# Performance work log

Measured on AMD Instinct MI355X. Metric: run time of the kernel, lower is better.

The kernel has to match this reference:

```python
import jax, jax.numpy as jnp
import numpy as np

DIM = 1024
DEPTH = 2
D_STATE = 16
EXPAND = 2            # standard Mamba expand factor -> d_inner = 2*dim
D_CONV = 4
DT_RANK = DIM // 16   # ceil(dim/16) = 64
D_INNER = DIM * EXPAND
BATCH = 2
SEQ = 1024


def setup_inputs() -> dict:
    key = jax.random.key(0)
    ks = jax.random.split(key, 8)
    def n(k, shape, scale):
        return jax.random.normal(k, shape, jnp.float32) * scale
    # A_log initialized as log(1..N) per channel (S4D-real init, as in mamba_ssm)
    A_log = jnp.tile(jnp.log(jnp.arange(1, D_STATE + 1, dtype=jnp.float32))[None, None, :],
                     (DEPTH, D_INNER, 1))
    return {
        "x": n(ks[0], (BATCH, SEQ, DIM), 1.0),
        "in_proj_w": n(ks[1], (DEPTH, 2 * D_INNER, DIM), DIM ** -0.5),
        "conv_w": n(ks[2], (DEPTH, D_INNER, D_CONV), D_CONV ** -0.5),
        "conv_b": jnp.zeros((DEPTH, D_INNER), jnp.float32),
        "x_proj_w": n(ks[3], (DEPTH, DT_RANK + 2 * D_STATE, D_INNER), D_INNER ** -0.5),
        "dt_proj_w": n(ks[4], (DEPTH, D_INNER, DT_RANK), DT_RANK ** -0.5),
        "dt_proj_b": n(ks[5], (DEPTH, D_INNER), 0.1),
        "A_log": A_log,
        "D": jnp.ones((DEPTH, D_INNER), jnp.float32),
        "out_proj_w": n(ks[6], (DEPTH, DIM, D_INNER), D_INNER ** -0.5),
    }


def _mamba_layer(x, in_w, cw, cb, xp_w, dtw, dtb, A_log, Dp, ow):
    # x: [B, L, dim]
    Bsz = x.shape[0]
    xz = jnp.einsum('bld,ed->ble', x, in_w)            # [B, L, 2*d_inner]
    xi, z = jnp.split(xz, 2, axis=-1)
    # causal depthwise conv1d over time
    xc = jnp.transpose(xi, (0, 2, 1))                  # [B, d_inner, L]
    xc = jax.lax.conv_general_dilated(xc, cw[:, None, :], (1,), [(D_CONV - 1, 0)],
                                      feature_group_count=D_INNER)
    xc = xc + cb[None, :, None]
    xc = jax.nn.silu(jnp.transpose(xc, (0, 2, 1)))     # [B, L, d_inner]
    # input-dependent dt, B, C
    x_dbl = jnp.einsum('bld,ed->ble', xc, xp_w)        # [B, L, dt_rank+2*N]
    dt_raw = x_dbl[..., :DT_RANK]
    Bm = x_dbl[..., DT_RANK:DT_RANK + D_STATE]         # [B, L, N]
    Cm = x_dbl[..., DT_RANK + D_STATE:]                # [B, L, N]
    dt = jax.nn.softplus(jnp.einsum('blr,dr->bld', dt_raw, dtw) + dtb)  # [B, L, d_inner]
    A = -jnp.exp(A_log)                                # [d_inner, N]
    dA = jnp.exp(dt[..., None] * A[None, None])        # [B, L, d_inner, N]
    dBu = dt[..., None] * Bm[:, :, None, :] * xc[..., None]

    def step(h, inp):
        dA_t, dBu_t, C_t = inp
        h = dA_t * h + dBu_t                           # [B, d_inner, N]
        y = jnp.einsum('bdn,bn->bd', h, C_t)
        return h, y

    h0 = jnp.zeros((Bsz, D_INNER, D_STATE), x.dtype)
    _, ys = jax.lax.scan(step, h0,
                         (dA.transpose(1, 0, 2, 3), dBu.transpose(1, 0, 2, 3),
                          Cm.transpose(1, 0, 2)))
    y = ys.transpose(1, 0, 2) + Dp[None, None, :] * xc
    y = y * jax.nn.silu(z)
    return jnp.einsum('bld,od->blo', y, ow)


def reference(x, in_proj_w, conv_w, conv_b, x_proj_w, dt_proj_w, dt_proj_b, A_log, D, out_proj_w):
    for i in range(DEPTH):
        x = _mamba_layer(x, in_proj_w[i], conv_w[i], conv_b[i], x_proj_w[i],
                         dt_proj_w[i], dt_proj_b[i], A_log[i], D[i], out_proj_w[i])
    return x
```

## Files before the change

kernel.cpp:

```cpp
#include <hip/hip_runtime.h>
#include <hip/hip_bf16.h>

typedef __hip_bfloat16 bf16;
typedef __attribute__((ext_vector_type(8))) short short8;
typedef __attribute__((ext_vector_type(4))) short shortx4;
typedef __attribute__((ext_vector_type(4))) float floatx4;

#define BATCH   2
#define SEQ     1024
#define DIM     1024
#define D_INNER 2048
#define D_STATE 16
#define DT_RANK 64
#define MROWS   (BATCH * SEQ)
#define CHUNK   32
#define NCHUNK  (SEQ / CHUNK)

__device__ __forceinline__ float bf2f(bf16 x) { return __bfloat162float(x); }
__device__ __forceinline__ bf16  f2bf(float x) { return __float2bfloat16(x); }
__device__ __forceinline__ short bfbits(float x) {
    bf16 b = __float2bfloat16(x); short s; __builtin_memcpy(&s, &b, 2); return s;
}

__device__ __forceinline__ void ld_lds16(const void* g, void* l) {
    __builtin_amdgcn_global_load_lds(
        (const __attribute__((address_space(1))) void*)g,
        (__attribute__((address_space(3))) void*)l, 16, 0, 0);
}

__device__ __forceinline__ void cast4(const float* in, short* o, int i) {
    floatx4 v = ((const floatx4*)in)[i];
    shortx4 r;
    r.x = bfbits(v.x); r.y = bfbits(v.y); r.z = bfbits(v.z); r.w = bfbits(v.w);
    ((shortx4*)o)[i] = r;
}
__global__ __launch_bounds__(256) void cast_k(
    const float* __restrict__ in, short* __restrict__ o, int n4)
{
    int i = blockIdx.x * 256 + threadIdx.x;
    if (i < n4) cast4(in, o, i);
}
__global__ __launch_bounds__(256) void cast2_k(
    const float* __restrict__ a, short* __restrict__ oa, int na4,
    const float* __restrict__ b, short* __restrict__ ob, int nb4)
{
    int i = blockIdx.x * 256 + threadIdx.x;
    if (i < na4) cast4(a, oa, i);
    else if (i - na4 < nb4) cast4(b, ob, i - na4);
}

__device__ __forceinline__ short8 ld8_any(const void* p, size_t eoff, int is_f32) {
    if (is_f32) {
        const float* f = (const float*)p + eoff;
        floatx4 a = *(const floatx4*)f;
        floatx4 b = *(const floatx4*)(f + 4);
        short8 r;
        r[0] = bfbits(a[0]); r[1] = bfbits(a[1]); r[2] = bfbits(a[2]); r[3] = bfbits(a[3]);
        r[4] = bfbits(b[0]); r[5] = bfbits(b[1]); r[6] = bfbits(b[2]); r[7] = bfbits(b[3]);
        return r;
    } else {
        return *(const short8*)((const bf16*)p + eoff);
    }
}

__global__ __launch_bounds__(256) void gemm128(
    const bf16* __restrict__ A, int lda,
    const bf16* __restrict__ B, int ldb,
    float* __restrict__ Cf, bf16* __restrict__ Cb, int ldc,
    int kchunk, size_t psize)
{
    __shared__ short As[128 * 32];
    __shared__ short Bs[128 * 32];
    const int tid  = threadIdx.x;
    const int wave = tid >> 6;
    const int lane = tid & 63;
    const int m0 = blockIdx.y * 128;
    const int n0 = blockIdx.x * 128;
    const int wm = (wave & 1) * 64;
    const int wn = (wave >> 1) * 64;
    const int r16  = lane & 15;
    const int quad = lane >> 4;
    const int r0 = tid >> 2;
    const int c0 = (tid & 3) << 3;
    const int kbeg = blockIdx.z * kchunk;

    floatx4 acc[4][4] = {};

    for (int k0 = kbeg; k0 < kbeg + kchunk; k0 += 32) {
        __syncthreads();
        ld_lds16(A + (size_t)(m0 + r0) * lda + k0 + c0,      As + tid * 8);
        ld_lds16(A + (size_t)(m0 + r0 + 64) * lda + k0 + c0, As + (tid + 256) * 8);
        ld_lds16(B + (size_t)(n0 + r0) * ldb + k0 + c0,      Bs + tid * 8);
        ld_lds16(B + (size_t)(n0 + r0 + 64) * ldb + k0 + c0, Bs + (tid + 256) * 8);
        __syncthreads();
        short8 af[4], bg[4];
#pragma unroll
        for (int i = 0; i < 4; i++) {
            af[i] = *(const short8*)(As + (wm + i * 16 + r16) * 32 + quad * 8);
            bg[i] = *(const short8*)(Bs + (wn + i * 16 + r16) * 32 + quad * 8);
        }
#pragma unroll
        for (int i = 0; i < 4; i++)
#pragma unroll
            for (int j = 0; j < 4; j++)
                acc[i][j] = __builtin_amdgcn_mfma_f32_16x16x32_bf16(af[i], bg[j], acc[i][j], 0, 0, 0);
    }

    float* Cfp = Cf ? Cf + (size_t)blockIdx.z * psize : nullptr;
#pragma unroll
    for (int i = 0; i < 4; i++)
#pragma unroll
        for (int j = 0; j < 4; j++) {
            int gm = m0 + wm + i * 16 + quad * 4;
            int gn = n0 + wn + j * 16 + r16;
#pragma unroll
            for (int r = 0; r < 4; r++) {
                size_t o = (size_t)(gm + r) * ldc + gn;
                float v = acc[i][j][r];
                if (Cfp) Cfp[o] = v;
                if (Cb) Cb[o] = f2bf(v);
            }
        }
}

__global__ __launch_bounds__(256) void gemm_bt(
    const void* __restrict__ A, int a_f32, int lda,
    const void* __restrict__ B, int b_f32, int ldb,
    float* __restrict__ Cf, bf16* __restrict__ Cb, int ldc,
    int N, int K, size_t psize,
    const float* __restrict__ bias, int act)
{
    __shared__ short As[64][40];
    __shared__ short Bs[64][40];
    const int m0   = blockIdx.y * 64;
    const int n0   = blockIdx.x * 64;
    const int tid  = threadIdx.x;
    const int wave = tid >> 6;
    const int lane = tid & 63;
    const int srow = tid >> 2;
    const int scol = (tid & 3) << 3;
    const int r16  = lane & 15;
    const int quad = lane >> 4;
    const int kbeg = blockIdx.z * K;

    floatx4 acc[4] = {};

    for (int k0 = kbeg; k0 < kbeg + K; k0 += 32) {
        short8 av = ld8_any(A, (size_t)(m0 + srow) * lda + k0 + scol, a_f32);
        short8 bv = {};
        int gn = n0 + srow;
        if (gn < N) bv = ld8_any(B, (size_t)gn * ldb + k0 + scol, b_f32);
        *(short8*)(&As[srow][scol]) = av;
        *(short8*)(&Bs[srow][scol]) = bv;
        __syncthreads();
        short8 af = *(const short8*)(&As[wave * 16 + r16][quad * 8]);
#pragma unroll
        for (int nt = 0; nt < 4; nt++) {
            short8 bq = *(const short8*)(&Bs[nt * 16 + r16][quad * 8]);
            acc[nt] = __builtin_amdgcn_mfma_f32_16x16x32_bf16(af, bq, acc[nt], 0, 0, 0);
        }
        __syncthreads();
    }

    float* Cfp = Cf ? Cf + (size_t)blockIdx.z * psize : nullptr;
#pragma unroll
    for (int nt = 0; nt < 4; nt++) {
        int gn = n0 + nt * 16 + r16;
        if (gn >= N) continue;
        float bsv = bias ? bias[gn] : 0.f;
#pragma unroll
        for (int r = 0; r < 4; r++) {
            int gm = m0 + wave * 16 + quad * 4 + r;
            float v = acc[nt][r] + bsv;
            if (act == 1) v = (v > 20.f) ? v : log1pf(__expf(v));
            size_t o = (size_t)gm * ldc + gn;
            if (Cfp) Cfp[o] = v;
            if (Cb) Cb[o] = f2bf(v);
        }
    }
}

__global__ __launch_bounds__(256) void reduce8_k(
    const float* __restrict__ part, float* __restrict__ o, int n, size_t psize)
{
    int i = blockIdx.x * 256 + threadIdx.x;
    if (i >= n) return;
    float v = 0.f;
#pragma unroll
    for (int j = 0; j < 8; j++) v += part[i + (size_t)j * psize];
    o[i] = v;
}

__global__ __launch_bounds__(256) void reduce2_k(
    const float* __restrict__ part, size_t psize, int n,
    float* __restrict__ of, bf16* __restrict__ ob)
{
    int i = blockIdx.x * 256 + threadIdx.x;
    if (i >= n) return;
    float v = part[i] + part[i + psize];
    if (of) of[i] = v;
    if (ob) ob[i] = f2bf(v);
}

__global__ __launch_bounds__(256) void conv_silu_k(
    const bf16* __restrict__ xz, const float* __restrict__ cw,
    const float* __restrict__ cb, bf16* __restrict__ xcb)
{
    int idx = blockIdx.x * 256 + threadIdx.x;
    int d   = idx & (D_INNER - 1);
    int bt  = idx >> 11;
    int t   = bt & (SEQ - 1);
    float s = cb[d];
#pragma unroll
    for (int j = 0; j < 4; j++) {
        int tt = t - 3 + j;
        if (tt >= 0) s += cw[d * 4 + j] * bf2f(xz[(size_t)(bt - 3 + j) * 4096 + d]);
    }
    float sig = 1.f / (1.f + __expf(-s));
    xcb[idx] = f2bf(s * sig);
}

__global__ __launch_bounds__(256) void scan1_k(
    const float* __restrict__ dtf, const bf16* __restrict__ xcb,
    const float* __restrict__ xdbl, const float* __restrict__ Alog,
    float* __restrict__ chunk_sdt, float* __restrict__ chunk_S)
{
    __shared__ float dt_s[CHUNK][256];
    __shared__ short xc_s[CHUNK][256];
    __shared__ float B_s[CHUNK][16];
    const int tid = threadIdx.x;
    const int d0  = blockIdx.x * 256;
    const int d   = d0 + tid;
    const int b   = blockIdx.y;
    const int c   = blockIdx.z;
    const size_t rbase = (size_t)b * SEQ + c * CHUNK;

#pragma unroll 4
    for (int t = 0; t < CHUNK; t++) {
        dt_s[t][tid] = dtf[(rbase + t) * D_INNER + d0 + tid];
        ((short*)xc_s)[t * 256 + tid] = *(const short*)&xcb[(rbase + t) * D_INNER + d0 + tid];
    }
    for (int e = tid; e < CHUNK * 16; e += 256) {
        int t = e >> 4, n = e & 15;
        B_s[t][n] = xdbl[(rbase + t) * 96 + 64 + n];
    }
    float A[16];
#pragma unroll
    for (int n = 0; n < 16; n++) A[n] = -__expf(Alog[(size_t)d * 16 + n]);
    float h[16] = {};
    float sdt = 0.f;
    __syncthreads();

    for (int t = 0; t < CHUNK; t++) {
        float dtv = dt_s[t][tid];
        bf16 xcr; short xs = xc_s[t][tid]; __builtin_memcpy(&xcr, &xs, 2);
        float u = dtv * bf2f(xcr);
        sdt += dtv;
        floatx4 B0 = *(const floatx4*)&B_s[t][0];
        floatx4 B1 = *(const floatx4*)&B_s[t][4];
        floatx4 B2 = *(const floatx4*)&B_s[t][8];
        floatx4 B3 = *(const floatx4*)&B_s[t][12];
#pragma unroll
        for (int n = 0; n < 4; n++) {
            h[n]      = __expf(dtv * A[n])      * h[n]      + u * B0[n];
            h[n + 4]  = __expf(dtv * A[n + 4])  * h[n + 4]  + u * B1[n];
            h[n + 8]  = __expf(dtv * A[n + 8])  * h[n + 8]  + u * B2[n];
            h[n + 12] = __expf(dtv * A[n + 12]) * h[n + 12] + u * B3[n];
        }
    }
    chunk_sdt[(b * NCHUNK + c) * D_INNER + d] = sdt;
#pragma unroll
    for (int n = 0; n < 16; n++)
        chunk_S[((size_t)(b * NCHUNK + c) * 16 + n) * D_INNER + d] = h[n];
}

__global__ __launch_bounds__(256) void scanpre_k(
    const float* __restrict__ Alog, const float* __restrict__ chunk_sdt,
    float* __restrict__ chunk_S)
{
    const int d = blockIdx.x * 256 + threadIdx.x;
    const int b = blockIdx.y;
    const int n = blockIdx.z;
    const float Av = -__expf(Alog[(size_t)d * 16 + n]);
    float h = 0.f;
    for (int j = 0; j < NCHUNK; j++) {
        size_t si = ((size_t)(b * NCHUNK + j) * 16 + n) * D_INNER + d;
        float S   = chunk_S[si];
        float sdt = chunk_sdt[(b * NCHUNK + j) * D_INNER + d];
        chunk_S[si] = h;
        h = __expf(sdt * Av) * h + S;
    }
}

__global__ __launch_bounds__(256) void scan2_k(
    const float* __restrict__ dtf, const bf16* __restrict__ xcb,
    const float* __restrict__ xdbl, const bf16* __restrict__ xz,
    const float* __restrict__ Alog, const float* __restrict__ Dp,
    const float* __restrict__ chunk_S, bf16* __restrict__ yb)
{
    __shared__ float dt_s[CHUNK][256];
    __shared__ short xc_s[CHUNK][256];
    __shared__ float B_s[CHUNK][16];
    __shared__ float C_s[CHUNK][16];
    const int tid = threadIdx.x;
    const int d0  = blockIdx.x * 256;
    const int d   = d0 + tid;
    const int b   = blockIdx.y;
    const int c   = blockIdx.z;
    const size_t rbase = (size_t)b * SEQ + c * CHUNK;

#pragma unroll 4
    for (int t = 0; t < CHUNK; t++) {
        dt_s[t][tid] = dtf[(rbase + t) * D_INNER + d0 + tid];
        ((short*)xc_s)[t * 256 + tid] = *(const short*)&xcb[(rbase + t) * D_INNER + d0 + tid];
    }
    for (int e = tid; e < CHUNK * 16; e += 256) {
        int t = e >> 4, n = e & 15;
        B_s[t][n] = xdbl[(rbase + t) * 96 + 64 + n];
        C_s[t][n] = xdbl[(rbase + t) * 96 + 80 + n];
    }
    float A[16];
#pragma unroll
    for (int n = 0; n < 16; n++) A[n] = -__expf(Alog[(size_t)d * 16 + n]);

    float h[16];
#pragma unroll
    for (int n = 0; n < 16; n++)
        h[n] = chunk_S[((size_t)(b * NCHUNK + c) * 16 + n) * D_INNER + d];

    const float Dv = Dp[d];
    __syncthreads();

    for (int t = 0; t < CHUNK; t++) {
        size_t row = rbase + t;
        float dtv = dt_s[t][tid];
        bf16 xcr; short xs = xc_s[t][tid]; __builtin_memcpy(&xcr, &xs, 2);
        float xcv = bf2f(xcr);
        float u = dtv * xcv;
        floatx4 B0 = *(const floatx4*)&B_s[t][0];
        floatx4 B1 = *(const floatx4*)&B_s[t][4];
        floatx4 B2 = *(const floatx4*)&B_s[t][8];
        floatx4 B3 = *(const floatx4*)&B_s[t][12];
        floatx4 C0 = *(const floatx4*)&C_s[t][0];
        floatx4 C1 = *(const floatx4*)&C_s[t][4];
        floatx4 C2 = *(const floatx4*)&C_s[t][8];
        floatx4 C3 = *(const floatx4*)&C_s[t][12];
        float y = 0.f;
#pragma unroll
        for (int n = 0; n < 4; n++) {
            h[n]      = __expf(dtv * A[n])      * h[n]      + u * B0[n];
            h[n + 4]  = __expf(dtv * A[n + 4])  * h[n + 4]  + u * B1[n];
            h[n + 8]  = __expf(dtv * A[n + 8])  * h[n + 8]  + u * B2[n];
            h[n + 12] = __expf(dtv * A[n + 12]) * h[n + 12] + u * B3[n];
            y += h[n] * C0[n] + h[n + 4] * C1[n] + h[n + 8] * C2[n] + h[n + 12] * C3[n];
        }
        float zv = bf2f(xz[row * 4096 + 2048 + d]);
        y = (y + Dv * xcv) * (zv / (1.f + __expf(-zv)));
        yb[row * D_INNER + d] = f2bf(y);
    }
}

extern "C" void kernel_launch(void* const* d_in, const int* in_sizes, int n_in,
                              void* d_out, int out_size, void* d_ws, size_t ws_size,
                              hipStream_t stream)
{
    const float* x    = (const float*)d_in[0];
    const float* inw  = (const float*)d_in[1];
    const float* cw   = (const float*)d_in[2];
    const float* cb   = (const float*)d_in[3];
    const float* xpw  = (const float*)d_in[4];
    const float* dtw  = (const float*)d_in[5];
    const float* dtb  = (const float*)d_in[6];
    const float* Alog = (const float*)d_in[7];
    const float* Dp   = (const float*)d_in[8];
    const float* ow   = (const float*)d_in[9];
    float* out = (float*)d_out;

    char* p = (char*)d_ws;
    bf16*  xzb   = (bf16*)p;  p += (size_t)MROWS * 4096 * 2;
    bf16*  xcb   = (bf16*)p;  p += (size_t)MROWS * D_INNER * 2;
    float* xdblf = (float*)p; p += (size_t)MROWS * 96 * 4;
    float* dtf   = (float*)p; p += (size_t)MROWS * D_INNER * 4;
    bf16*  ybf   = (bf16*)p;  p += (size_t)MROWS * D_INNER * 2;
    bf16*  xmid  = (bf16*)p;  p += (size_t)MROWS * DIM * 2;
    float* csdt  = (float*)p; p += (size_t)BATCH * NCHUNK * D_INNER * 4;
    float* cS    = (float*)p; p += (size_t)BATCH * NCHUNK * 16 * D_INNER * 4;
    bf16*  xb    = (bf16*)p;  p += (size_t)MROWS * DIM * 2;
    bf16*  inwb  = (bf16*)p;  p += (size_t)2 * D_INNER * DIM * 2;
    bf16*  owb   = (bf16*)p;  p += (size_t)DIM * D_INNER * 2;
    float* xprt  = (float*)p; p += (size_t)8 * MROWS * 96 * 4;

    const size_t xp_psize = (size_t)MROWS * 96;
    const size_t op_psize = (size_t)MROWS * DIM;
    float* outp = dtf;

    cast_k<<<(MROWS * DIM / 4 + 255) / 256, 256, 0, stream>>>(x, (short*)xb, MROWS * DIM / 4);

    for (int l = 0; l < 2; l++) {
        const float* xpw_l = xpw + (size_t)l * 96 * D_INNER;
        const float* dtw_l = dtw + (size_t)l * D_INNER * DT_RANK;
        const float* Al    = Alog + (size_t)l * D_INNER * D_STATE;

        {
            int na4 = 2 * D_INNER * DIM / 4, nb4 = DIM * D_INNER / 4;
            cast2_k<<<(na4 + nb4 + 255) / 256, 256, 0, stream>>>(
                inw + (size_t)l * 2 * D_INNER * DIM, (short*)inwb, na4,
                ow + (size_t)l * DIM * D_INNER, (short*)owb, nb4);
        }

        gemm128<<<dim3(32, 16, 1), 256, 0, stream>>>(
            (l == 0) ? xb : xmid, DIM, inwb, DIM,
            nullptr, xzb, 4096, DIM, 0);

        conv_silu_k<<<(MROWS * D_INNER) / 256, 256, 0, stream>>>(
            xzb, cw + (size_t)l * D_INNER * 4, cb + (size_t)l * D_INNER, xcb);

        gemm_bt<<<dim3(2, 32, 8), 256, 0, stream>>>(
            xcb, 0, D_INNER, xpw_l, 1, D_INNER,
            xprt, nullptr, 96, 96, 256, xp_psize, nullptr, 0);
        reduce8_k<<<(MROWS * 96 + 255) / 256, 256, 0, stream>>>(
            xprt, xdblf, MROWS * 96, xp_psize);

        gemm_bt<<<dim3(32, 32), 256, 0, stream>>>(
            xdblf, 1, 96, dtw_l, 1, DT_RANK,
            dtf, nullptr, D_INNER, D_INNER, DT_RANK, 0,
            dtb + (size_t)l * D_INNER, 1);

        scan1_k<<<dim3(D_INNER / 256, BATCH, NCHUNK), 256, 0, stream>>>(
            dtf, xcb, xdblf, Al, csdt, cS);
        scanpre_k<<<dim3(D_INNER / 256, BATCH, D_STATE), 256, 0, stream>>>(
            Al, csdt, cS);
        scan2_k<<<dim3(D_INNER / 256, BATCH, NCHUNK), 256, 0, stream>>>(
            dtf, xcb, xdblf, xzb, Al, Dp + (size_t)l * D_INNER, cS, ybf);

        gemm128<<<dim3(8, 16, 2), 256, 0, stream>>>(
            ybf, D_INNER, owb, D_INNER,
            outp, nullptr, DIM, D_INNER / 2, op_psize);
        reduce2_k<<<(MROWS * DIM + 255) / 256, 256, 0, stream>>>(
            outp, op_psize, MROWS * DIM,
            (l == 1) ? out : nullptr, (l == 0) ? xmid : nullptr);
    }
}
```

Measured before the change: 445.6 us.

## Multi-stage async LDS pipeline with swizzle in gemm128; split-K 4 for out_proj

Turns the gemm128 main loop into a 4-buffer, prefetch-distance-2 pipeline. Direct-to-LDS loads are tracked with explicit vmcnt waits and a single barrier per k-step, and MFMA runs at raised priority. It adds an XOR swizzle on the LDS columns to reduce bank conflicts. Out_proj split-K goes from 2 to 4 with a generic reduce kernel, which gives more blocks for parallelism but more partial-sum traffic. The LDS footprint grows fourfold, which may lower occupancy.

```diff
diff --git a/kernel.cpp b/kernel.cpp
--- a/kernel.cpp
+++ b/kernel.cpp
@@ -69,8 +69,8 @@
     float* __restrict__ Cf, bf16* __restrict__ Cb, int ldc,
     int kchunk, size_t psize)
 {
-    __shared__ short As[128 * 32];
-    __shared__ short Bs[128 * 32];
+    __shared__ short As[4][128 * 32];
+    __shared__ short Bs[4][128 * 32];
     const int tid  = threadIdx.x;
     const int wave = tid >> 6;
     const int lane = tid & 63;
@@ -80,31 +80,57 @@
     const int wn = (wave >> 1) * 64;
     const int r16  = lane & 15;
     const int quad = lane >> 4;
-    const int r0 = tid >> 2;
-    const int c0 = (tid & 3) << 3;
+    const int r0   = tid >> 2;
+    const int csw   = (((tid & 3) ^ ((r0 >> 1) & 3)) << 3);
+    const int swoff = ((quad ^ ((r16 >> 1) & 3)) << 3);
     const int kbeg = blockIdx.z * kchunk;
+    const int nk   = kchunk >> 5;
 
     floatx4 acc[4][4] = {};
 
-    for (int k0 = kbeg; k0 < kbeg + kchunk; k0 += 32) {
-        __syncthreads();
-        ld_lds16(A + (size_t)(m0 + r0) * lda + k0 + c0,      As + tid * 8);
-        ld_lds16(A + (size_t)(m0 + r0 + 64) * lda + k0 + c0, As + (tid + 256) * 8);
-        ld_lds16(B + (size_t)(n0 + r0) * ldb + k0 + c0,      Bs + tid * 8);
-        ld_lds16(B + (size_t)(n0 + r0 + 64) * ldb + k0 + c0, Bs + (tid + 256) * 8);
-        __syncthreads();
+    auto STAGE = [&](int buf, int kk) {
+        ld_lds16(A + (size_t)(m0 + r0) * lda + kk + csw,      &As[buf][tid * 8]);
+        ld_lds16(A + (size_t)(m0 + r0 + 64) * lda + kk + csw, &As[buf][(tid + 256) * 8]);
+        ld_lds16(B + (size_t)(n0 + r0) * ldb + kk + csw,      &Bs[buf][tid * 8]);
+        ld_lds16(B + (size_t)(n0 + r0 + 64) * ldb + kk + csw, &Bs[buf][(tid + 256) * 8]);
+    };
+    auto COMPUTE = [&](int buf) {
+        const short* Ab = As[buf];
+        const short* Bb = Bs[buf];
         short8 af[4], bg[4];
 #pragma unroll
         for (int i = 0; i < 4; i++) {
-            af[i] = *(const short8*)(As + (wm + i * 16 + r16) * 32 + quad * 8);
-            bg[i] = *(const short8*)(Bs + (wn + i * 16 + r16) * 32 + quad * 8);
-        }
+            af[i] = *(const short8*)(Ab + (wm + i * 16 + r16) * 32 + swoff);
+            bg[i] = *(const short8*)(Bb + (wn + i * 16 + r16) * 32 + swoff);
+        }
+        __builtin_amdgcn_s_setprio(1);
 #pragma unroll
         for (int i = 0; i < 4; i++)
 #pragma unroll
             for (int j = 0; j < 4; j++)
                 acc[i][j] = __builtin_amdgcn_mfma_f32_16x16x32_bf16(af[i], bg[j], acc[i][j], 0, 0, 0);
-    }
+        __builtin_amdgcn_s_setprio(0);
+    };
+
+    STAGE(0, kbeg);
+    STAGE(1, kbeg + 32);
+    int it = 0;
+    for (; it < nk - 2; ++it) {
+        STAGE((it + 2) & 3, kbeg + (it + 2) * 32);
+        asm volatile("s_waitcnt vmcnt(8) lgkmcnt(0)" ::: "memory");
+        __builtin_amdgcn_s_barrier();
+        __builtin_amdgcn_sched_barrier(0);
+        COMPUTE(it & 3);
+    }
+    asm volatile("s_waitcnt vmcnt(4) lgkmcnt(0)" ::: "memory");
+    __builtin_amdgcn_s_barrier();
+    __builtin_amdgcn_sched_barrier(0);
+    COMPUTE(it & 3);
+    ++it;
+    asm volatile("s_waitcnt vmcnt(0) lgkmcnt(0)" ::: "memory");
+    __builtin_amdgcn_s_barrier();
+    __builtin_amdgcn_sched_barrier(0);
+    COMPUTE(it & 3);
 
     float* Cfp = Cf ? Cf + (size_t)blockIdx.z * psize : nullptr;
 #pragma unroll
@@ -180,24 +206,14 @@
     }
 }
 
-__global__ __launch_bounds__(256) void reduce8_k(
-    const float* __restrict__ part, float* __restrict__ o, int n, size_t psize)
+__global__ __launch_bounds__(256) void reduceN_k(
+    const float* __restrict__ part, size_t psize, int n, int np,
+    float* __restrict__ of, bf16* __restrict__ ob)
 {
     int i = blockIdx.x * 256 + threadIdx.x;
     if (i >= n) return;
     float v = 0.f;
-#pragma unroll
-    for (int j = 0; j < 8; j++) v += part[i + (size_t)j * psize];
-    o[i] = v;
-}
-
-__global__ __launch_bounds__(256) void reduce2_k(
-    const float* __restrict__ part, size_t psize, int n,
-    float* __restrict__ of, bf16* __restrict__ ob)
-{
-    int i = blockIdx.x * 256 + threadIdx.x;
-    if (i >= n) return;
-    float v = part[i] + part[i + psize];
+    for (int j = 0; j < np; j++) v += part[i + (size_t)j * psize];
     if (of) of[i] = v;
     if (ob) ob[i] = f2bf(v);
 }
@@ -389,10 +405,10 @@
     bf16*  inwb  = (bf16*)p;  p += (size_t)2 * D_INNER * DIM * 2;
     bf16*  owb   = (bf16*)p;  p += (size_t)DIM * D_INNER * 2;
     float* xprt  = (float*)p; p += (size_t)8 * MROWS * 96 * 4;
+    float* oprt  = (float*)p; p += (size_t)4 * MROWS * DIM * 4;
 
     const size_t xp_psize = (size_t)MROWS * 96;
     const size_t op_psize = (size_t)MROWS * DIM;
-    float* outp = dtf;
 
     cast_k<<<(MROWS * DIM / 4 + 255) / 256, 256, 0, stream>>>(x, (short*)xb, MROWS * DIM / 4);
 
@@ -418,8 +434,8 @@
         gemm_bt<<<dim3(2, 32, 8), 256, 0, stream>>>(
             xcb, 0, D_INNER, xpw_l, 1, D_INNER,
             xprt, nullptr, 96, 96, 256, xp_psize, nullptr, 0);
-        reduce8_k<<<(MROWS * 96 + 255) / 256, 256, 0, stream>>>(
-            xprt, xdblf, MROWS * 96, xp_psize);
+        reduceN_k<<<(MROWS * 96 + 255) / 256, 256, 0, stream>>>(
+            xprt, xp_psize, MROWS * 96, 8, xdblf, nullptr);
 
         gemm_bt<<<dim3(32, 32), 256, 0, stream>>>(
             xdblf, 1, 96, dtw_l, 1, DT_RANK,
@@ -433,11 +449,11 @@
         scan2_k<<<dim3(D_INNER / 256, BATCH, NCHUNK), 256, 0, stream>>>(
             dtf, xcb, xdblf, xzb, Al, Dp + (size_t)l * D_INNER, cS, ybf);
 
-        gemm128<<<dim3(8, 16, 2), 256, 0, stream>>>(
+        gemm128<<<dim3(8, 16, 4), 256, 0, stream>>>(
             ybf, D_INNER, owb, D_INNER,
-            outp, nullptr, DIM, D_INNER / 2, op_psize);
-        reduce2_k<<<(MROWS * DIM + 255) / 256, 256, 0, stream>>>(
-            outp, op_psize, MROWS * DIM,
+            oprt, nullptr, DIM, D_INNER / 4, op_psize);
+        reduceN_k<<<(MROWS * DIM + 255) / 256, 256, 0, stream>>>(
+            oprt, op_psize, MROWS * DIM, 4,
             (l == 1) ? out : nullptr, (l == 0) ? xmid : nullptr);
     }
 }
```

Measured after the change: 422.7 us. 5.1% less time.
